# Optimization experiments

Hardware: AMD Instinct MI355X
Metric: run time of the kernel (lower is better)

The kernel has to match this reference:

```python
import jax, jax.numpy as jnp
import numpy as np

N_NODES = 50000
N_EDGES = 800000
D_NODE = 128
D_EDGE = 16
HID = 64
EPS = 1e-5


def _sage_conv(x, src, dst, Wl, bl, Wr, n_nodes):
    # PyG SAGEConv (mean aggr): out = lin_l(mean_{src->dst} x[src]) + lin_r(x)
    msg = x[src]                                        # [E, F] gather
    s = jax.ops.segment_sum(msg, dst, num_segments=n_nodes)   # [N, F]
    cnt = jax.ops.segment_sum(jnp.ones((src.shape[0],), x.dtype), dst,
                              num_segments=n_nodes)
    agg = s / jnp.maximum(cnt, 1.0)[:, None]
    return agg @ Wl.T + bl + x @ Wr.T


def _batchnorm(h, gamma, beta):
    # training-mode BN over node dim (biased variance, as in torch)
    mu = jnp.mean(h, axis=0)
    var = jnp.mean((h - mu) ** 2, axis=0)
    return gamma * (h - mu) / jnp.sqrt(var + EPS) + beta


def setup_inputs() -> dict:
    key = jax.random.key(0)
    ks = jax.random.split(key, 16)
    def lin(k, out_f, in_f):
        lim = 1.0 / np.sqrt(in_f)
        return jax.random.uniform(k, (out_f, in_f), jnp.float32, -lim, lim)
    x = jax.random.normal(ks[0], (N_NODES, D_NODE), jnp.float32)
    edge_index = jax.random.randint(ks[1], (2, N_EDGES), 0, N_NODES, jnp.int64)
    edge_attr = jax.random.normal(ks[2], (N_EDGES, D_EDGE), jnp.float32)
    return {
        "x": x, "edge_index": edge_index, "edge_attr": edge_attr,
        # SAGEConv 1
        "W1l": lin(ks[3], HID, D_NODE), "b1l": jnp.zeros((HID,), jnp.float32),
        "W1r": lin(ks[4], HID, D_NODE),
        "g1": jnp.ones((HID,), jnp.float32), "be1": jnp.zeros((HID,), jnp.float32),
        # SAGEConv 2
        "W2l": lin(ks[5], HID, HID), "b2l": jnp.zeros((HID,), jnp.float32),
        "W2r": lin(ks[6], HID, HID),
        "g2": jnp.ones((HID,), jnp.float32), "be2": jnp.zeros((HID,), jnp.float32),
        # edge MLP: (2*HID + D_EDGE) -> 128 -> 64 -> 2
        "Wm1": lin(ks[7], 128, 2 * HID + D_EDGE), "bm1": jnp.zeros((128,), jnp.float32),
        "Wm2": lin(ks[8], 64, 128), "bm2": jnp.zeros((64,), jnp.float32),
        "Wm3": lin(ks[9], 2, 64), "bm3": jnp.zeros((2,), jnp.float32),
    }


def reference(x, edge_index, edge_attr,
              W1l, b1l, W1r, g1, be1,
              W2l, b2l, W2r, g2, be2,
              Wm1, bm1, Wm2, bm2, Wm3, bm3):
    src, dst = edge_index[0], edge_index[1]
    n = x.shape[0]
    h = _sage_conv(x, src, dst, W1l, b1l, W1r, n)
    h = jax.nn.relu(_batchnorm(h, g1, be1))          # dropout = identity (eval)
    h = _sage_conv(h, src, dst, W2l, b2l, W2r, n)
    h = jax.nn.relu(_batchnorm(h, g2, be2))
    edge_in = jnp.concatenate([h[src], edge_attr, h[dst]], axis=1)  # [E, 144]
    z = jax.nn.relu(edge_in @ Wm1.T + bm1)
    z = jax.nn.relu(z @ Wm2.T + bm2)
    return z @ Wm3.T + bm3                           # [E, 2] logits
```

## Files before the change

### kernel.cpp

```cpp
#include <hip/hip_runtime.h>
#include <hip/hip_fp16.h>


#define EPS 1e-5f

typedef _Float16 h8 __attribute__((ext_vector_type(8)));
typedef float f32x4 __attribute__((ext_vector_type(4)));

__global__ __launch_bounds__(256) void k_prep_hist(
    const float* __restrict__ W1l, const float* __restrict__ W1r,
    const float* __restrict__ b1l,
    const float* __restrict__ W2l, const float* __restrict__ W2r,
    const float* __restrict__ b2l,
    const float* __restrict__ Wm1, const float* __restrict__ Wm2,
    float* __restrict__ Wt1, float* __restrict__ Wt2,
    float* __restrict__ bias1, float* __restrict__ bias2,
    __half* __restrict__ W2B, __half* __restrict__ W1B,
    const int* __restrict__ dst, int* __restrict__ deg, int E, int prepBlocks) {
  if ((int)blockIdx.x >= prepBlocks) {
    int e = (blockIdx.x - prepBlocks) * 256 + threadIdx.x;
    if (e < E) atomicAdd(&deg[dst[e]], 1);
    return;
  }
  int idx = blockIdx.x * 256 + threadIdx.x;
  if (idx < 16384) {
    int k = idx >> 7, f = idx & 127;
    Wt1[idx] = (f < 64) ? W1l[f * 128 + k] : W1r[(f - 64) * 128 + k];
    return;
  }
  idx -= 16384;
  if (idx < 8192) {
    int k = idx >> 7, f = idx & 127;
    Wt2[idx] = (f < 64) ? W2l[f * 64 + k] : W2r[(f - 64) * 64 + k];
    return;
  }
  idx -= 8192;
  if (idx < 128) { bias1[idx] = (idx < 64) ? 0.f : b1l[idx - 64]; return; }
  idx -= 128;
  if (idx < 128) { bias2[idx] = (idx < 64) ? 0.f : b2l[idx - 64]; return; }
  idx -= 128;
  if (idx < 8192) {
    int j = idx & 7, l = (idx >> 3) & 63, f = idx >> 9;
    int kc = f >> 2, tt = f & 3;
    int col = 16 * tt + (l & 15);
    int k = 32 * kc + (l >> 4) * 8 + j;
    W2B[idx] = __float2half(Wm2[col * 128 + k]);
    return;
  }
  idx -= 8192;
  if (idx < 20480) {
    int j = idx & 7, l = (idx >> 3) & 63, f = idx >> 9;
    int kc = f >> 3, nc = f & 7;
    int k = 32 * kc + (l >> 4) * 8 + j;
    int n = 16 * nc + (l & 15);
    float w;
    if (k < 64)       w = Wm1[n * 144 + k];
    else if (k < 128) w = Wm1[n * 144 + 80 + (k - 64)];
    else if (k < 144) w = Wm1[n * 144 + 64 + (k - 128)];
    else              w = 0.f;
    W1B[idx] = __float2half(w);
    return;
  }
}

__global__ __launch_bounds__(1024) void k_scan(
    const int* __restrict__ deg, int* __restrict__ rowptr,
    int* __restrict__ cursor, int N) {
  __shared__ int wsum[16];
  __shared__ int carry;
  const int lane = threadIdx.x & 63;
  const int w    = threadIdx.x >> 6;
  if (threadIdx.x == 0) carry = 0;
  __syncthreads();
  for (int base = 0; base < N; base += 1024) {
    int i = base + threadIdx.x;
    int v = (i < N) ? deg[i] : 0;
    int incl = v;
#pragma unroll
    for (int off = 1; off < 64; off <<= 1) {
      int t = __shfl_up(incl, off);
      if (lane >= off) incl += t;
    }
    if (lane == 63) wsum[w] = incl;
    __syncthreads();
    if (w == 0) {
      int ws_ = (lane < 16) ? wsum[lane] : 0;
      int wincl = ws_;
#pragma unroll
      for (int off = 1; off < 16; off <<= 1) {
        int t = __shfl_up(wincl, off);
        if (lane >= off) wincl += t;
      }
      if (lane < 16) wsum[lane] = wincl;
    }
    __syncthreads();
    int woff = carry + (w > 0 ? wsum[w - 1] : 0);
    int excl = woff + incl - v;
    if (i < N) { rowptr[i] = excl; cursor[i] = excl; }
    int tot = wsum[15];
    __syncthreads();
    if (threadIdx.x == 0) carry += tot;
    __syncthreads();
  }
  if (threadIdx.x == 0) rowptr[N] = carry;
}

__global__ __launch_bounds__(256) void k_fill(
    const int* __restrict__ src, const int* __restrict__ dst,
    const float* __restrict__ attr,
    int* __restrict__ cursor, int* __restrict__ csr_src,
    int* __restrict__ csr_dst, int* __restrict__ pos,
    __half* __restrict__ attrC, int E) {
  int e = blockIdx.x * 256 + threadIdx.x;
  if (e < E) {
    int d = dst[e];
    int p = atomicAdd(&cursor[d], 1);
    csr_src[p] = src[e];
    csr_dst[p] = d;
    pos[e] = p;
    const float4* at4 = (const float4*)attr;
    float4 a0 = at4[(size_t)e * 4 + 0];
    float4 a1 = at4[(size_t)e * 4 + 1];
    float4 a2 = at4[(size_t)e * 4 + 2];
    float4 a3 = at4[(size_t)e * 4 + 3];
    __half2 hh[8];
    hh[0] = __floats2half2_rn(a0.x, a0.y);
    hh[1] = __floats2half2_rn(a0.z, a0.w);
    hh[2] = __floats2half2_rn(a1.x, a1.y);
    hh[3] = __floats2half2_rn(a1.z, a1.w);
    hh[4] = __floats2half2_rn(a2.x, a2.y);
    hh[5] = __floats2half2_rn(a2.z, a2.w);
    hh[6] = __floats2half2_rn(a3.x, a3.y);
    hh[7] = __floats2half2_rn(a3.z, a3.w);
    *(uint4*)&attrC[(size_t)p * 16]     = *(uint4*)&hh[0];
    *(uint4*)&attrC[(size_t)p * 16 + 8] = *(uint4*)&hh[4];
  }
}

__global__ __launch_bounds__(256) void k_scatter_out(
    const float* __restrict__ out2, const int* __restrict__ pos,
    float* __restrict__ out, int E) {
  int e = blockIdx.x * 256 + threadIdx.x;
  if (e < E) {
    int p = pos[e];
    *(float2*)&out[(size_t)e * 2] = *(const float2*)&out2[(size_t)p * 2];
  }
}

template<int K, int MODE>
__global__ __launch_bounds__(256) void k_gemm(
    const float* __restrict__ X, const float* __restrict__ stats,
    const float* __restrict__ Wt, const float* __restrict__ bias,
    __half* __restrict__ outH, float* __restrict__ outF, int N, int Ftot) {
  __shared__ __align__(16) float Xs[32][68];
  __shared__ __align__(16) float Ws_[32][128];
  const int tid = threadIdx.x;
  const int tx  = tid & 15;
  const int ty  = tid >> 4;
  const int n0  = blockIdx.x * 64;
  float acc[4][8];
#pragma unroll
  for (int j = 0; j < 8; ++j) {
    float bv = bias[8 * tx + j];
#pragma unroll
    for (int i = 0; i < 4; ++i) acc[i][j] = bv;
  }
  for (int k0 = 0; k0 < K; k0 += 32) {
    __syncthreads();
#pragma unroll
    for (int l = 0; l < 2; ++l) {
      int idx = tid * 2 + l;
      int kq = idx & 7, n = idx >> 3;
      float4 xv = make_float4(0.f, 0.f, 0.f, 0.f);
      if (n0 + n < N) xv = *(const float4*)&X[(size_t)(n0 + n) * K + k0 + kq * 4];
      if (stats) {
        int kb = k0 + kq * 4;
        xv.x = fmaxf(xv.x * stats[128 + kb + 0] + stats[192 + kb + 0], 0.f);
        xv.y = fmaxf(xv.y * stats[128 + kb + 1] + stats[192 + kb + 1], 0.f);
        xv.z = fmaxf(xv.z * stats[128 + kb + 2] + stats[192 + kb + 2], 0.f);
        xv.w = fmaxf(xv.w * stats[128 + kb + 3] + stats[192 + kb + 3], 0.f);
      }
      Xs[kq * 4 + 0][n] = xv.x;
      Xs[kq * 4 + 1][n] = xv.y;
      Xs[kq * 4 + 2][n] = xv.z;
      Xs[kq * 4 + 3][n] = xv.w;
    }
#pragma unroll
    for (int l = 0; l < 4; ++l) {
      int idx = tid + l * 256;
      int kr = idx >> 5, fc = idx & 31;
      *(float4*)&Ws_[kr][fc * 4] =
          *(const float4*)&Wt[(size_t)(k0 + kr) * Ftot + fc * 4];
    }
    __syncthreads();
#pragma unroll
    for (int kk = 0; kk < 32; ++kk) {
      float4 a  = *(const float4*)&Xs[kk][4 * ty];
      float4 b0 = *(const float4*)&Ws_[kk][8 * tx];
      float4 b1 = *(const float4*)&Ws_[kk][8 * tx + 4];
      float aa[4] = {a.x, a.y, a.z, a.w};
      float bb[8] = {b0.x, b0.y, b0.z, b0.w, b1.x, b1.y, b1.z, b1.w};
#pragma unroll
      for (int i = 0; i < 4; ++i)
#pragma unroll
        for (int j = 0; j < 8; ++j) acc[i][j] += aa[i] * bb[j];
    }
  }
#pragma unroll
  for (int i = 0; i < 4; ++i) {
    int n = n0 + 4 * ty + i;
    if (n >= N) continue;
    if (tx < 8) {
      __half2 hh[4];
#pragma unroll
      for (int c = 0; c < 4; ++c)
        hh[c] = __floats2half2_rn(acc[i][2 * c], acc[i][2 * c + 1]);
      *(uint4*)&outH[(size_t)n * 64 + 8 * tx] = *(uint4*)hh;
    } else {
      float* cp = outF + (size_t)n * 64 + 8 * tx - 64;
      *(float4*)cp = make_float4(acc[i][0], acc[i][1], acc[i][2], acc[i][3]);
      *(float4*)(cp + 4) = make_float4(acc[i][4], acc[i][5], acc[i][6], acc[i][7]);
    }
  }
}

__global__ __launch_bounds__(256) void k_agg(
    const __half* __restrict__ qb, const float* __restrict__ pb,
    const int* __restrict__ rowptr, const int* __restrict__ csr_src,
    float* __restrict__ hpre, float* __restrict__ stats, int N) {
  __shared__ float red[512];
  const int tid  = threadIdx.x;
  const int w    = tid >> 6;
  const int lane = tid & 63;
  const int g    = lane >> 3, c = lane & 7;
  float lsum = 0.f, lsq = 0.f;
  const int wid = blockIdx.x * 4 + w;
  const int nw  = gridDim.x * 4;
  for (int n = wid; n < N; n += nw) {
    const int r0 = rowptr[n], r1 = rowptr[n + 1];
    float s[8] = {0.f, 0.f, 0.f, 0.f, 0.f, 0.f, 0.f, 0.f};
    for (int j = r0 + g; j < r1; j += 8) {
      int a = csr_src[j];
      uint4 rv = *(const uint4*)&qb[(size_t)a * 64 + 8 * c];
      const __half2* hp = (const __half2*)&rv;
#pragma unroll
      for (int q = 0; q < 4; ++q) {
        float2 f2 = __half22float2(hp[q]);
        s[2 * q]     += f2.x;
        s[2 * q + 1] += f2.y;
      }
    }
#pragma unroll
    for (int m = 8; m < 64; m <<= 1)
#pragma unroll
      for (int q = 0; q < 8; ++q) s[q] += __shfl_xor(s[q], m);
    float sv = s[0];
#pragma unroll
    for (int q = 1; q < 8; ++q) sv = (g == q) ? s[q] : sv;
    float cdeg = (float)(r1 - r0);
    cdeg = cdeg > 1.f ? cdeg : 1.f;
    const int f = 8 * c + g;
    float v = sv / cdeg + pb[(size_t)n * 64 + f];
    hpre[(size_t)n * 64 + f] = v;
    lsum += v;
    lsq  += v * v;
  }
  red[tid]       = lsum;
  red[256 + tid] = lsq;
  __syncthreads();
  if (tid < 64) {
    float ts = red[tid] + red[tid + 64] + red[tid + 128] + red[tid + 192];
    float tq = red[256 + tid] + red[256 + tid + 64] + red[256 + tid + 128] + red[256 + tid + 192];
    int f = 8 * (tid & 7) + (tid >> 3);
    atomicAdd(&stats[f], ts);
    atomicAdd(&stats[64 + f], tq);
  }
}

__global__ void k_finalize(float* stats, const float* __restrict__ g,
                           const float* __restrict__ be, int N) {
  int f = threadIdx.x;
  float inv_n = 1.0f / (float)N;
  float mean = stats[f] * inv_n;
  float var  = stats[64 + f] * inv_n - mean * mean;
  float s = g[f] * rsqrtf(var + EPS);
  stats[128 + f] = s;
  stats[192 + f] = be[f] - mean * s;
}

__global__ __launch_bounds__(256) void k_bn(
    const float* __restrict__ H1, const float* __restrict__ stats,
    __half* __restrict__ H2, int N) {
  int idx = blockIdx.x * 256 + threadIdx.x;
  if (idx >= N * 8) return;
  int n = idx >> 3, f8 = (idx & 7) * 8;
  float4 h0 = *(const float4*)&H1[(size_t)n * 64 + f8];
  float4 h1 = *(const float4*)&H1[(size_t)n * 64 + f8 + 4];
  const float* sc = stats + 128 + f8;
  const float* sh = stats + 192 + f8;
  __half2 hh[4];
  hh[0] = __floats2half2_rn(fmaxf(h0.x * sc[0] + sh[0], 0.f),
                            fmaxf(h0.y * sc[1] + sh[1], 0.f));
  hh[1] = __floats2half2_rn(fmaxf(h0.z * sc[2] + sh[2], 0.f),
                            fmaxf(h0.w * sc[3] + sh[3], 0.f));
  hh[2] = __floats2half2_rn(fmaxf(h1.x * sc[4] + sh[4], 0.f),
                            fmaxf(h1.y * sc[5] + sh[5], 0.f));
  hh[3] = __floats2half2_rn(fmaxf(h1.z * sc[6] + sh[6], 0.f),
                            fmaxf(h1.w * sc[7] + sh[7], 0.f));
  *(uint4*)&H2[(size_t)n * 64 + f8] = *(uint4*)hh;
}

__global__ __launch_bounds__(256, 2) void k_edge(
    const __half* __restrict__ H2, const __half* __restrict__ attrC,
    const int* __restrict__ csrc, const int* __restrict__ cdst,
    const __half* __restrict__ W1Bws, const __half* __restrict__ W2Bws,
    const float* __restrict__ bm1, const float* __restrict__ bm2,
    const float* __restrict__ Wm3, const float* __restrict__ bm3,
    float* __restrict__ out2, int E) {
  __shared__ __align__(16) _Float16 W1B[20480];
  __shared__ __align__(16) _Float16 W2B[8192];
  __shared__ __align__(16) _Float16 Z1f[64 * 136];

  const int tid  = threadIdx.x;
  const int lane = tid & 63;
  const int w    = tid >> 6;
  const int ln15 = lane & 15;
  const int quad = lane >> 4;

  for (int i = tid; i < 2560; i += 256)
    ((uint4*)W1B)[i] = ((const uint4*)W1Bws)[i];
  for (int i = tid; i < 1024; i += 256)
    ((uint4*)W2B)[i] = ((const uint4*)W2Bws)[i];

  float bm1v[8];
#pragma unroll
  for (int nc = 0; nc < 8; ++nc) bm1v[nc] = bm1[16 * nc + ln15];
  float bmv[4], w30[4], w31[4];
#pragma unroll
  for (int t = 0; t < 4; ++t) {
    bmv[t] = bm2[16 * t + ln15];
    w30[t] = Wm3[16 * t + ln15];
    w31[t] = Wm3[64 + 16 * t + ln15];
  }
  const float bm30 = bm3[0], bm31 = bm3[1];
  __syncthreads();

  const int nt = (E + 63) >> 6;
  const int rowoff = 16 * w + ln15;

  for (int t = blockIdx.x; t < nt; t += gridDim.x) {
    int er = (t << 6) + rowoff;
    if (er >= E) er = E - 1;
    const int s = csrc[er];
    const int d = cdst[er];

    h8 af0 = *(const h8*)&H2[(size_t)s * 64 + 8 * quad];
    h8 af1 = *(const h8*)&H2[(size_t)s * 64 + 32 + 8 * quad];
    h8 af2 = *(const h8*)&H2[(size_t)d * 64 + 8 * quad];
    h8 af3 = *(const h8*)&H2[(size_t)d * 64 + 32 + 8 * quad];
    h8 af4 = (h8){0, 0, 0, 0, 0, 0, 0, 0};
    if (quad < 2)
      af4 = *(const h8*)&attrC[(size_t)er * 16 + 8 * quad];

    const int ebase = 16 * w + 4 * quad;
#pragma unroll
    for (int nc = 0; nc < 8; ++nc) {
      f32x4 a1 = (f32x4){bm1v[nc], bm1v[nc], bm1v[nc], bm1v[nc]};
      a1 = __builtin_amdgcn_mfma_f32_16x16x32_f16(
          af0, *(const h8*)&W1B[((0 * 8 + nc) << 9) + (lane << 3)], a1, 0, 0, 0);
      a1 = __builtin_amdgcn_mfma_f32_16x16x32_f16(
          af1, *(const h8*)&W1B[((1 * 8 + nc) << 9) + (lane << 3)], a1, 0, 0, 0);
      a1 = __builtin_amdgcn_mfma_f32_16x16x32_f16(
          af2, *(const h8*)&W1B[((2 * 8 + nc) << 9) + (lane << 3)], a1, 0, 0, 0);
      a1 = __builtin_amdgcn_mfma_f32_16x16x32_f16(
          af3, *(const h8*)&W1B[((3 * 8 + nc) << 9) + (lane << 3)], a1, 0, 0, 0);
      a1 = __builtin_amdgcn_mfma_f32_16x16x32_f16(
          af4, *(const h8*)&W1B[((4 * 8 + nc) << 9) + (lane << 3)], a1, 0, 0, 0);
      Z1f[(ebase + 0) * 136 + 16 * nc + ln15] = (_Float16)fmaxf(a1[0], 0.f);
      Z1f[(ebase + 1) * 136 + 16 * nc + ln15] = (_Float16)fmaxf(a1[1], 0.f);
      Z1f[(ebase + 2) * 136 + 16 * nc + ln15] = (_Float16)fmaxf(a1[2], 0.f);
      Z1f[(ebase + 3) * 136 + 16 * nc + ln15] = (_Float16)fmaxf(a1[3], 0.f);
    }

    f32x4 acc2[4];
#pragma unroll
    for (int tt = 0; tt < 4; ++tt)
      acc2[tt] = (f32x4){bmv[tt], bmv[tt], bmv[tt], bmv[tt]};
#pragma unroll
    for (int kc = 0; kc < 4; ++kc) {
      h8 a = *(const h8*)&Z1f[(16 * w + ln15) * 136 + 32 * kc + 8 * quad];
#pragma unroll
      for (int tt = 0; tt < 4; ++tt) {
        h8 bf = *(const h8*)&W2B[((kc * 4 + tt) * 64 + lane) * 8];
        acc2[tt] = __builtin_amdgcn_mfma_f32_16x16x32_f16(a, bf, acc2[tt], 0, 0, 0);
      }
    }

    float p0[4], p1[4];
#pragma unroll
    for (int r = 0; r < 4; ++r) { p0[r] = 0.f; p1[r] = 0.f; }
#pragma unroll
    for (int tt = 0; tt < 4; ++tt)
#pragma unroll
      for (int r = 0; r < 4; ++r) {
        float z = fmaxf(acc2[tt][r], 0.f);
        p0[r] += z * w30[tt];
        p1[r] += z * w31[tt];
      }
#pragma unroll
    for (int r = 0; r < 4; ++r) {
#pragma unroll
      for (int m = 1; m < 16; m <<= 1) {
        p0[r] += __shfl_xor(p0[r], m);
        p1[r] += __shfl_xor(p1[r], m);
      }
      if (ln15 == 0) {
        int j = (t << 6) + 16 * w + 4 * quad + r;
        if (j < E)
          *(float2*)&out2[(size_t)j * 2] = make_float2(p0[r] + bm30, p1[r] + bm31);
      }
    }
  }
}

extern "C" void kernel_launch(void* const* d_in, const int* in_sizes, int n_in,
                              void* d_out, int out_size, void* d_ws, size_t ws_size,
                              hipStream_t stream) {
  const float* x    = (const float*)d_in[0];
  const int*   ei   = (const int*)d_in[1];
  const float* attr = (const float*)d_in[2];
  const float* W1l  = (const float*)d_in[3];
  const float* b1l  = (const float*)d_in[4];
  const float* W1r  = (const float*)d_in[5];
  const float* g1   = (const float*)d_in[6];
  const float* be1  = (const float*)d_in[7];
  const float* W2l  = (const float*)d_in[8];
  const float* b2l  = (const float*)d_in[9];
  const float* W2r  = (const float*)d_in[10];
  const float* g2   = (const float*)d_in[11];
  const float* be2  = (const float*)d_in[12];
  const float* Wm1  = (const float*)d_in[13];
  const float* bm1  = (const float*)d_in[14];
  const float* Wm2  = (const float*)d_in[15];
  const float* bm2  = (const float*)d_in[16];
  const float* Wm3  = (const float*)d_in[17];
  const float* bm3  = (const float*)d_in[18];
  float* out = (float*)d_out;

  const int N = in_sizes[0] / 128;
  const int E = in_sizes[1] / 2;
  const int* srcI = ei;
  const int* dstI = ei + E;

  float* ws = (float*)d_ws;
  const size_t NF = (size_t)N * 64;
  float*  P32 = ws;
  float*  H1  = ws + NF;
  __half* Q16 = (__half*)(ws + 2 * NF);
  float* small  = ws + 2 * NF + NF / 2;
  float* stats1 = small;
  float* stats2 = stats1 + 256;
  float* Wt1    = stats2 + 256;
  float* Wt2    = Wt1 + 16384;
  float* bias1  = Wt2 + 8192;
  float* bias2  = bias1 + 128;
  __half* W1B   = (__half*)(bias2 + 128);
  __half* W2B   = (__half*)(bias2 + 128 + 10240);
  int* rowptr = (int*)(bias2 + 128 + 10240 + 4096);
  int* cursor = rowptr + (N + 1);
  int* deg    = cursor + N;
  int* csrsrc = deg + N;
  int* csrdst = csrsrc + E;
  int* pos    = csrdst + E;
  __half* attrC = (__half*)(pos + E);

  __half* H2  = Q16;
  float* out2 = H1;

  hipMemsetAsync(deg, 0, (size_t)N * sizeof(int), stream);
  hipMemsetAsync(stats1, 0, 512 * sizeof(float), stream);

  const int eBlocks = (E + 255) / 256;
  const int prepBlocks = (53504 + 255) / 256;
  k_prep_hist<<<prepBlocks + eBlocks, 256, 0, stream>>>(
      W1l, W1r, b1l, W2l, W2r, b2l, Wm1, Wm2,
      Wt1, Wt2, bias1, bias2, W2B, W1B,
      dstI, deg, E, prepBlocks);
  k_scan<<<1, 1024, 0, stream>>>(deg, rowptr, cursor, N);
  k_fill<<<eBlocks, 256, 0, stream>>>(srcI, dstI, attr, cursor,
                                      csrsrc, csrdst, pos, attrC, E);

  const int mTiles = (N + 63) / 64;

  k_gemm<128, 0><<<mTiles, 256, 0, stream>>>(x, nullptr, Wt1, bias1, Q16, P32, N, 128);
  k_agg<<<1024, 256, 0, stream>>>(Q16, P32, rowptr, csrsrc, H1, stats1, N);
  k_finalize<<<1, 64, 0, stream>>>(stats1, g1, be1, N);

  k_gemm<64, 0><<<mTiles, 256, 0, stream>>>(H1, stats1, Wt2, bias2, Q16, P32, N, 128);
  k_agg<<<1024, 256, 0, stream>>>(Q16, P32, rowptr, csrsrc, H1, stats2, N);
  k_finalize<<<1, 64, 0, stream>>>(stats2, g2, be2, N);

  k_bn<<<(N * 8 + 255) / 256, 256, 0, stream>>>(H1, stats2, H2, N);

  k_edge<<<1024, 256, 0, stream>>>(H2, attrC, csrsrc, csrdst,
                                   W1B, W2B, bm1, bm2, Wm3, bm3, out2, E);
  k_scatter_out<<<eBlocks, 256, 0, stream>>>(out2, pos, out, E);
}
```

Baseline: 539.7 us.

## Fold BN finalize into consumers, pack CSR src/dst, prefetch edge indices

Removes the two single-block finalize kernels by computing BatchNorm scale and shift into shared memory at the start of the second GEMM and the BN kernel. Packs the CSR source and destination arrays into one int2 array and has the edge MLP kernel prefetch the next tile's index pair. The aim is to cut launch overhead and serial tiny kernels, and to hide index-load latency in the edge kernel. In exchange, every block recomputes the 64 statistics, and the aggregation kernel now reads 8-byte entries where it only needs 4.

Result: no change. 540.1 us (+0.1%).

```diff
diff --git a/kernel.cpp b/kernel.cpp
--- a/kernel.cpp
+++ b/kernel.cpp
@@ -108,15 +108,13 @@
 __global__ __launch_bounds__(256) void k_fill(
     const int* __restrict__ src, const int* __restrict__ dst,
     const float* __restrict__ attr,
-    int* __restrict__ cursor, int* __restrict__ csr_src,
-    int* __restrict__ csr_dst, int* __restrict__ pos,
-    __half* __restrict__ attrC, int E) {
+    int* __restrict__ cursor, int2* __restrict__ csr_sd,
+    int* __restrict__ pos, __half* __restrict__ attrC, int E) {
   int e = blockIdx.x * 256 + threadIdx.x;
   if (e < E) {
     int d = dst[e];
     int p = atomicAdd(&cursor[d], 1);
-    csr_src[p] = src[e];
-    csr_dst[p] = d;
+    csr_sd[p] = make_int2(src[e], d);
     pos[e] = p;
     const float4* at4 = (const float4*)attr;
     float4 a0 = at4[(size_t)e * 4 + 0];
@@ -150,14 +148,24 @@
 template<int K, int MODE>
 __global__ __launch_bounds__(256) void k_gemm(
     const float* __restrict__ X, const float* __restrict__ stats,
+    const float* __restrict__ gma, const float* __restrict__ bta,
     const float* __restrict__ Wt, const float* __restrict__ bias,
     __half* __restrict__ outH, float* __restrict__ outF, int N, int Ftot) {
   __shared__ __align__(16) float Xs[32][68];
   __shared__ __align__(16) float Ws_[32][128];
+  __shared__ float scs[64], shs[64];
   const int tid = threadIdx.x;
   const int tx  = tid & 15;
   const int ty  = tid >> 4;
   const int n0  = blockIdx.x * 64;
+  if (stats && tid < 64) {
+    float inv_n = 1.0f / (float)N;
+    float mean = stats[tid] * inv_n;
+    float var  = stats[64 + tid] * inv_n - mean * mean;
+    float s = gma[tid] * rsqrtf(var + EPS);
+    scs[tid] = s;
+    shs[tid] = bta[tid] - mean * s;
+  }
   float acc[4][8];
 #pragma unroll
   for (int j = 0; j < 8; ++j) {
@@ -175,10 +183,10 @@
       if (n0 + n < N) xv = *(const float4*)&X[(size_t)(n0 + n) * K + k0 + kq * 4];
       if (stats) {
         int kb = k0 + kq * 4;
-        xv.x = fmaxf(xv.x * stats[128 + kb + 0] + stats[192 + kb + 0], 0.f);
-        xv.y = fmaxf(xv.y * stats[128 + kb + 1] + stats[192 + kb + 1], 0.f);
-        xv.z = fmaxf(xv.z * stats[128 + kb + 2] + stats[192 + kb + 2], 0.f);
-        xv.w = fmaxf(xv.w * stats[128 + kb + 3] + stats[192 + kb + 3], 0.f);
+        xv.x = fmaxf(xv.x * scs[kb + 0] + shs[kb + 0], 0.f);
+        xv.y = fmaxf(xv.y * scs[kb + 1] + shs[kb + 1], 0.f);
+        xv.z = fmaxf(xv.z * scs[kb + 2] + shs[kb + 2], 0.f);
+        xv.w = fmaxf(xv.w * scs[kb + 3] + shs[kb + 3], 0.f);
       }
       Xs[kq * 4 + 0][n] = xv.x;
       Xs[kq * 4 + 1][n] = xv.y;
@@ -226,7 +234,7 @@
 
 __global__ __launch_bounds__(256) void k_agg(
     const __half* __restrict__ qb, const float* __restrict__ pb,
-    const int* __restrict__ rowptr, const int* __restrict__ csr_src,
+    const int* __restrict__ rowptr, const int2* __restrict__ csr_sd,
     float* __restrict__ hpre, float* __restrict__ stats, int N) {
   __shared__ float red[512];
   const int tid  = threadIdx.x;
@@ -240,7 +248,7 @@
     const int r0 = rowptr[n], r1 = rowptr[n + 1];
     float s[8] = {0.f, 0.f, 0.f, 0.f, 0.f, 0.f, 0.f, 0.f};
     for (int j = r0 + g; j < r1; j += 8) {
-      int a = csr_src[j];
+      int a = csr_sd[j].x;
       uint4 rv = *(const uint4*)&qb[(size_t)a * 64 + 8 * c];
       const __half2* hp = (const __half2*)&rv;
 #pragma unroll
@@ -277,42 +285,41 @@
   }
 }
 
-__global__ void k_finalize(float* stats, const float* __restrict__ g,
-                           const float* __restrict__ be, int N) {
-  int f = threadIdx.x;
-  float inv_n = 1.0f / (float)N;
-  float mean = stats[f] * inv_n;
-  float var  = stats[64 + f] * inv_n - mean * mean;
-  float s = g[f] * rsqrtf(var + EPS);
-  stats[128 + f] = s;
-  stats[192 + f] = be[f] - mean * s;
-}
-
 __global__ __launch_bounds__(256) void k_bn(
     const float* __restrict__ H1, const float* __restrict__ stats,
+    const float* __restrict__ g, const float* __restrict__ be,
     __half* __restrict__ H2, int N) {
-  int idx = blockIdx.x * 256 + threadIdx.x;
+  __shared__ float scs[64], shs[64];
+  const int tid = threadIdx.x;
+  if (tid < 64) {
+    float inv_n = 1.0f / (float)N;
+    float mean = stats[tid] * inv_n;
+    float var  = stats[64 + tid] * inv_n - mean * mean;
+    float s = g[tid] * rsqrtf(var + EPS);
+    scs[tid] = s;
+    shs[tid] = be[tid] - mean * s;
+  }
+  __syncthreads();
+  int idx = blockIdx.x * 256 + tid;
   if (idx >= N * 8) return;
   int n = idx >> 3, f8 = (idx & 7) * 8;
   float4 h0 = *(const float4*)&H1[(size_t)n * 64 + f8];
   float4 h1 = *(const float4*)&H1[(size_t)n * 64 + f8 + 4];
-  const float* sc = stats + 128 + f8;
-  const float* sh = stats + 192 + f8;
   __half2 hh[4];
-  hh[0] = __floats2half2_rn(fmaxf(h0.x * sc[0] + sh[0], 0.f),
-                            fmaxf(h0.y * sc[1] + sh[1], 0.f));
-  hh[1] = __floats2half2_rn(fmaxf(h0.z * sc[2] + sh[2], 0.f),
-                            fmaxf(h0.w * sc[3] + sh[3], 0.f));
-  hh[2] = __floats2half2_rn(fmaxf(h1.x * sc[4] + sh[4], 0.f),
-                            fmaxf(h1.y * sc[5] + sh[5], 0.f));
-  hh[3] = __floats2half2_rn(fmaxf(h1.z * sc[6] + sh[6], 0.f),
-                            fmaxf(h1.w * sc[7] + sh[7], 0.f));
+  hh[0] = __floats2half2_rn(fmaxf(h0.x * scs[f8 + 0] + shs[f8 + 0], 0.f),
+                            fmaxf(h0.y * scs[f8 + 1] + shs[f8 + 1], 0.f));
+  hh[1] = __floats2half2_rn(fmaxf(h0.z * scs[f8 + 2] + shs[f8 + 2], 0.f),
+                            fmaxf(h0.w * scs[f8 + 3] + shs[f8 + 3], 0.f));
+  hh[2] = __floats2half2_rn(fmaxf(h1.x * scs[f8 + 4] + shs[f8 + 4], 0.f),
+                            fmaxf(h1.y * scs[f8 + 5] + shs[f8 + 5], 0.f));
+  hh[3] = __floats2half2_rn(fmaxf(h1.z * scs[f8 + 6] + shs[f8 + 6], 0.f),
+                            fmaxf(h1.w * scs[f8 + 7] + shs[f8 + 7], 0.f));
   *(uint4*)&H2[(size_t)n * 64 + f8] = *(uint4*)hh;
 }
 
 __global__ __launch_bounds__(256, 2) void k_edge(
     const __half* __restrict__ H2, const __half* __restrict__ attrC,
-    const int* __restrict__ csrc, const int* __restrict__ cdst,
+    const int2* __restrict__ csd,
     const __half* __restrict__ W1Bws, const __half* __restrict__ W2Bws,
     const float* __restrict__ bm1, const float* __restrict__ bm2,
     const float* __restrict__ Wm3, const float* __restrict__ bm3,
@@ -346,13 +353,22 @@
   __syncthreads();
 
   const int nt = (E + 63) >> 6;
+  const int G  = gridDim.x;
   const int rowoff = 16 * w + ln15;
 
-  for (int t = blockIdx.x; t < nt; t += gridDim.x) {
-    int er = (t << 6) + rowoff;
-    if (er >= E) er = E - 1;
-    const int s = csrc[er];
-    const int d = cdst[er];
+  int er0 = (blockIdx.x << 6) + rowoff;
+  if (er0 >= E) er0 = E - 1;
+  int2 sd = csd[er0];
+
+  for (int t = blockIdx.x; t < nt; t += G) {
+    int erN = ((t + G) << 6) + rowoff;
+    if (erN >= E) erN = E - 1;
+    int2 sdN = csd[erN];
+
+    int erc = (t << 6) + rowoff;
+    if (erc >= E) erc = E - 1;
+    const int s = sd.x;
+    const int d = sd.y;
 
     h8 af0 = *(const h8*)&H2[(size_t)s * 64 + 8 * quad];
     h8 af1 = *(const h8*)&H2[(size_t)s * 64 + 32 + 8 * quad];
@@ -360,7 +376,7 @@
     h8 af3 = *(const h8*)&H2[(size_t)d * 64 + 32 + 8 * quad];
     h8 af4 = (h8){0, 0, 0, 0, 0, 0, 0, 0};
     if (quad < 2)
-      af4 = *(const h8*)&attrC[(size_t)er * 16 + 8 * quad];
+      af4 = *(const h8*)&attrC[(size_t)erc * 16 + 8 * quad];
 
     const int ebase = 16 * w + 4 * quad;
 #pragma unroll
@@ -420,6 +436,8 @@
           *(float2*)&out2[(size_t)j * 2] = make_float2(p0[r] + bm30, p1[r] + bm31);
       }
     }
+
+    sd = sdN;
   }
 }
 
@@ -466,13 +484,12 @@
   float* bias2  = bias1 + 128;
   __half* W1B   = (__half*)(bias2 + 128);
   __half* W2B   = (__half*)(bias2 + 128 + 10240);
-  int* rowptr = (int*)(bias2 + 128 + 10240 + 4096);
+  int2* csr_sd = (int2*)(bias2 + 128 + 10240 + 4096);
+  int* rowptr = (int*)(csr_sd + E);
   int* cursor = rowptr + (N + 1);
   int* deg    = cursor + N;
-  int* csrsrc = deg + N;
-  int* csrdst = csrsrc + E;
-  int* pos    = csrdst + E;
-  __half* attrC = (__half*)(pos + E);
+  int* pos    = deg + N;
+  __half* attrC = (__half*)(((uintptr_t)(pos + E) + 15) & ~(uintptr_t)15);
 
   __half* H2  = Q16;
   float* out2 = H1;
@@ -488,21 +505,21 @@
       dstI, deg, E, prepBlocks);
   k_scan<<<1, 1024, 0, stream>>>(deg, rowptr, cursor, N);
   k_fill<<<eBlocks, 256, 0, stream>>>(srcI, dstI, attr, cursor,
-                                      csrsrc, csrdst, pos, attrC, E);
+                                      csr_sd, pos, attrC, E);
 
   const int mTiles = (N + 63) / 64;
 
-  k_gemm<128, 0><<<mTiles, 256, 0, stream>>>(x, nullptr, Wt1, bias1, Q16, P32, N, 128);
-  k_agg<<<1024, 256, 0, stream>>>(Q16, P32, rowptr, csrsrc, H1, stats1, N);
-  k_finalize<<<1, 64, 0, stream>>>(stats1, g1, be1, N);
-
-  k_gemm<64, 0><<<mTiles, 256, 0, stream>>>(H1, stats1, Wt2, bias2, Q16, P32, N, 128);
-  k_agg<<<1024, 256, 0, stream>>>(Q16, P32, rowptr, csrsrc, H1, stats2, N);
-  k_finalize<<<1, 64, 0, stream>>>(stats2, g2, be2, N);
-
-  k_bn<<<(N * 8 + 255) / 256, 256, 0, stream>>>(H1, stats2, H2, N);
-
-  k_edge<<<1024, 256, 0, stream>>>(H2, attrC, csrsrc, csrdst,
+  k_gemm<128, 0><<<mTiles, 256, 0, stream>>>(x, nullptr, nullptr, nullptr,
+                                             Wt1, bias1, Q16, P32, N, 128);
+  k_agg<<<1024, 256, 0, stream>>>(Q16, P32, rowptr, csr_sd, H1, stats1, N);
+
+  k_gemm<64, 0><<<mTiles, 256, 0, stream>>>(H1, stats1, g1, be1,
+                                            Wt2, bias2, Q16, P32, N, 128);
+  k_agg<<<1024, 256, 0, stream>>>(Q16, P32, rowptr, csr_sd, H1, stats2, N);
+
+  k_bn<<<(N * 8 + 255) / 256, 256, 0, stream>>>(H1, stats2, g2, be2, H2, N);
+
+  k_edge<<<1024, 256, 0, stream>>>(H2, attrC, csr_sd,
                                    W1B, W2B, bm1, bm2, Wm3, bm3, out2, E);
   k_scatter_out<<<eBlocks, 256, 0, stream>>>(out2, pos, out, E);
 }
```
